# Kernel optimization log

Hardware: AMD Instinct MI355X
Metric: run time of the kernel (lower is better)

Reference implementation:

```python
import jax, jax.numpy as jnp
import numpy as np

N_NODES = 100000


def setup_inputs() -> dict:
    key = jax.random.key(0)
    ks = jax.random.split(key, 8)
    IN, HID, OUT = 128, 128, 64
    E = 1600000
    x = jax.random.normal(ks[0], (N_NODES, IN), dtype=jnp.float32)
    edge_index = jax.random.randint(ks[1], (2, E), 0, N_NODES, dtype=jnp.int64)
    # PyG SAGEConv params: lin_l (applied to aggregated neighbors, with bias),
    # lin_r (root weight, no bias).
    def lin(k, fi, fo):
        return jax.random.normal(k, (fi, fo), dtype=jnp.float32) / np.sqrt(fi)
    Wl0 = lin(ks[2], IN, HID)
    bl0 = jnp.zeros((HID,), dtype=jnp.float32)
    Wr0 = lin(ks[3], IN, HID)
    Wl1 = lin(ks[4], HID, OUT)
    bl1 = jnp.zeros((OUT,), dtype=jnp.float32)
    Wr1 = lin(ks[5], HID, OUT)
    return {"x": x, "edge_index": edge_index,
            "Wl0": Wl0, "bl0": bl0, "Wr0": Wr0,
            "Wl1": Wl1, "bl1": bl1, "Wr1": Wr1}


def _sage_conv(h, src, dst, Wl, bl, Wr):
    # mean aggregation of source features onto target nodes
    summed = jax.ops.segment_sum(h[src], dst, num_segments=N_NODES)  # [N, d]
    cnt = jax.ops.segment_sum(jnp.ones((src.shape[0], 1), h.dtype), dst,
                              num_segments=N_NODES)                  # [N, 1]
    agg = summed / jnp.maximum(cnt, 1.0)
    return agg @ Wl + bl + h @ Wr


def reference(x, edge_index, Wl0, bl0, Wr0, Wl1, bl1, Wr1):
    src, dst = edge_index[0], edge_index[1]
    h = jax.nn.relu(_sage_conv(x, src, dst, Wl0, bl0, Wr0))
    # dropout is identity in eval mode (training=False)
    return _sage_conv(h, src, dst, Wl1, bl1, Wr1)
```

## Files before the change

kernel.cpp:

```cpp
#include <hip/hip_runtime.h>


typedef short short8 __attribute__((ext_vector_type(8)));
typedef float f32x4 __attribute__((ext_vector_type(4)));
typedef float f32x2 __attribute__((ext_vector_type(2)));

#define NBUCK 782
#define BCAP  3072
#define EPB   8192

static __device__ __forceinline__ unsigned short f2bf(float f) {
    union { float f; unsigned u; } c; c.f = f;
    unsigned u = c.u + 0x7fffu + ((c.u >> 16) & 1u);
    return (unsigned short)(u >> 16);
}
static __device__ __forceinline__ float bf2f(unsigned short b) {
    union { unsigned u; float f; } c; c.u = ((unsigned)b) << 16;
    return c.f;
}
static __device__ __forceinline__ float bf2f_s(short b) {
    return bf2f((unsigned short)b);
}

static __device__ __forceinline__ unsigned char f2fp8(float x) {
    union { float f; unsigned u; } c; c.f = x;
    unsigned s = (c.u >> 24) & 0x80u;
    float a = __builtin_fabsf(x);
    if (a < 0.015625f) {
        int m = (int)rintf(a * 512.0f);
        return (unsigned char)(s | (unsigned)m);
    }
    unsigned u = c.u + 0x7ffffu + ((c.u >> 20) & 1u);
    int e = (int)((u >> 23) & 0xff) - 120;
    unsigned m = (u >> 20) & 7u;
    if (e > 15) { e = 15; m = 6; }
    return (unsigned char)(s | (unsigned)(e << 3) | m);
}

static __device__ __forceinline__ void acc_fp8x4(unsigned w, float* a) {
#if __has_builtin(__builtin_amdgcn_cvt_pk_f32_fp8)
    f32x2 lo = __builtin_amdgcn_cvt_pk_f32_fp8((int)w, false);
    f32x2 hi = __builtin_amdgcn_cvt_pk_f32_fp8((int)w, true);
    a[0] += lo[0]; a[1] += lo[1]; a[2] += hi[0]; a[3] += hi[1];
#else
    #pragma unroll
    for (int j = 0; j < 4; ++j) {
        unsigned b = (w >> (8 * j)) & 0xffu;
        union { unsigned u; float f; } c;
        c.u = ((b & 0x80u) << 24) | ((b & 0x7fu) << 20);
        a[j] += c.f * 0x1p120f;
    }
#endif
}
static __device__ __forceinline__ void acc_row16(uint4 w, float* a) {
    acc_fp8x4(w.x, a + 0);  acc_fp8x4(w.y, a + 4);
    acc_fp8x4(w.z, a + 8);  acc_fp8x4(w.w, a + 12);
}

__global__ __launch_bounds__(256) void k_pack(const float* __restrict__ WA,
                                              const float* __restrict__ WB,
                                              int CA, int NC,
                                              unsigned short* __restrict__ Wp) {
    int tid = blockIdx.x * 256 + threadIdx.x;
    if (tid >= NC * 16) return;
    int lane = tid & 63, kk = (tid >> 6) & 3, tg = tid >> 8;
    int l15 = lane & 15, quad = lane >> 4;
    int c = tg * 16 + l15;
    const float* W = (c < CA) ? WA : WB;
    int cc = (c < CA) ? c : c - CA;
    short8 v;
    #pragma unroll
    for (int j = 0; j < 8; ++j) {
        int k = kk * 32 + quad * 8 + j;
        v[j] = (short)f2bf(W[(size_t)k * CA + cc]);
    }
    *(short8*)(Wp + (size_t)tid * 8) = v;
}

__global__ __launch_bounds__(256) void k_gemm0_bucket(
        const float* __restrict__ X, const unsigned short* __restrict__ Wp,
        unsigned char* __restrict__ P0, unsigned short* __restrict__ Q0, int Nrows,
        const int* __restrict__ src, const int* __restrict__ dst,
        int* __restrict__ cursor, int* __restrict__ bregion,
        int E, int gemmBlocks) {
    const int t = threadIdx.x;
    if ((int)blockIdx.x < gemmBlocks) {
        const int wave = t >> 6, lane = t & 63;
        const int quad = lane >> 4, l15 = lane & 15;
        const int row0 = blockIdx.x * 32;
        const int c0w = wave * 64;
        f32x4 acc[2][4];
        #pragma unroll
        for (int mt = 0; mt < 2; ++mt)
            #pragma unroll
            for (int tt = 0; tt < 4; ++tt) acc[mt][tt] = (f32x4){0.f, 0.f, 0.f, 0.f};
        #pragma unroll
        for (int kk = 0; kk < 4; ++kk) {
            const int k0 = kk * 32 + quad * 8;
            short8 a[2];
            #pragma unroll
            for (int mt = 0; mt < 2; ++mt) {
                int row = row0 + mt * 16 + l15;
                if (row > Nrows - 1) row = Nrows - 1;
                const float* xp = X + (size_t)row * 128 + k0;
                float4 f0 = *(const float4*)xp;
                float4 f1 = *(const float4*)(xp + 4);
                short8 v;
                v[0] = (short)f2bf(f0.x); v[1] = (short)f2bf(f0.y);
                v[2] = (short)f2bf(f0.z); v[3] = (short)f2bf(f0.w);
                v[4] = (short)f2bf(f1.x); v[5] = (short)f2bf(f1.y);
                v[6] = (short)f2bf(f1.z); v[7] = (short)f2bf(f1.w);
                a[mt] = v;
            }
            short8 b[4];
            #pragma unroll
            for (int tt = 0; tt < 4; ++tt) {
                int tg = (c0w >> 4) + tt;
                b[tt] = *(const short8*)(Wp + ((size_t)(tg * 4 + kk) * 64 + lane) * 8);
            }
            #pragma unroll
            for (int mt = 0; mt < 2; ++mt)
                #pragma unroll
                for (int tt = 0; tt < 4; ++tt)
                    acc[mt][tt] = __builtin_amdgcn_mfma_f32_16x16x32_bf16(
                        a[mt], b[tt], acc[mt][tt], 0, 0, 0);
        }
        #pragma unroll
        for (int mt = 0; mt < 2; ++mt)
            #pragma unroll
            for (int r = 0; r < 4; ++r) {
                int row = row0 + mt * 16 + quad * 4 + r;
                if (row < Nrows) {
                    if (c0w < 128) {
                        #pragma unroll
                        for (int tt = 0; tt < 4; ++tt)
                            P0[(size_t)row * 128 + c0w + tt * 16 + l15] =
                                f2fp8(acc[mt][tt][r]);
                    } else {
                        #pragma unroll
                        for (int tt = 0; tt < 4; ++tt)
                            Q0[(size_t)row * 128 + (c0w - 128) + tt * 16 + l15] =
                                f2bf(acc[mt][tt][r]);
                    }
                }
            }
        return;
    }
    __shared__ int hist[NBUCK];
    __shared__ int basel[NBUCK];
    int bid = blockIdx.x - gemmBlocks;
    for (int i = t; i < NBUCK; i += 256) hist[i] = 0;
    __syncthreads();
    int e0 = bid * EPB + t * 32;
    int d[32];
    if (e0 + 32 <= E) {
        #pragma unroll
        for (int q = 0; q < 8; ++q) {
            int4 v = *(const int4*)(dst + e0 + q * 4);
            d[q * 4 + 0] = v.x; d[q * 4 + 1] = v.y;
            d[q * 4 + 2] = v.z; d[q * 4 + 3] = v.w;
        }
    } else {
        #pragma unroll
        for (int j = 0; j < 32; ++j) d[j] = (e0 + j < E) ? dst[e0 + j] : -1;
    }
    #pragma unroll
    for (int j = 0; j < 32; ++j)
        if (d[j] >= 0) atomicAdd(&hist[d[j] >> 7], 1);
    __syncthreads();
    for (int i = t; i < NBUCK; i += 256) {
        int c = hist[i];
        basel[i] = (c > 0) ? atomicAdd(&cursor[i], c) : 0;
    }
    __syncthreads();
    for (int i = t; i < NBUCK; i += 256) hist[i] = 0;
    __syncthreads();
    int s[32];
    if (e0 + 32 <= E) {
        #pragma unroll
        for (int q = 0; q < 8; ++q) {
            int4 v = *(const int4*)(src + e0 + q * 4);
            s[q * 4 + 0] = v.x; s[q * 4 + 1] = v.y;
            s[q * 4 + 2] = v.z; s[q * 4 + 3] = v.w;
        }
    } else {
        #pragma unroll
        for (int j = 0; j < 32; ++j) s[j] = (e0 + j < E) ? src[e0 + j] : 0;
    }
    #pragma unroll
    for (int j = 0; j < 32; ++j) {
        if (d[j] < 0) continue;
        int b = d[j] >> 7;
        int r = atomicAdd(&hist[b], 1);
        bregion[(size_t)b * BCAP + basel[b] + r] = s[j] | ((d[j] & 127) << 20);
    }
}

__global__ __launch_bounds__(256) void k_csr(const int* __restrict__ cursor,
                                             const int* __restrict__ bregion,
                                             int* __restrict__ rowptr,
                                             int* __restrict__ csr, int Nn) {
    __shared__ int words[BCAP];
    __shared__ int hist[128], sc[128], rank[128];
    __shared__ int red[256];
    int b = blockIdx.x, t = threadIdx.x;
    int part = 0;
    for (int i = t; i < b; i += 256) part += cursor[i];
    red[t] = part;
    if (t < 128) { hist[t] = 0; rank[t] = 0; }
    __syncthreads();
    #pragma unroll
    for (int off = 128; off > 0; off >>= 1) {
        if (t < off) red[t] += red[t + off];
        __syncthreads();
    }
    int gbase = red[0];
    int cnt = cursor[b];
    for (int i = t; i < cnt; i += 256) {
        int w = bregion[(size_t)b * BCAP + i];
        words[i] = w;
        atomicAdd(&hist[w >> 20], 1);
    }
    __syncthreads();
    if (t < 128) sc[t] = hist[t];
    __syncthreads();
    #pragma unroll
    for (int off = 1; off < 128; off <<= 1) {
        int x = 0;
        if (t < 128 && t >= off) x = sc[t - off];
        __syncthreads();
        if (t < 128) sc[t] += x;
        __syncthreads();
    }
    if (t < 128) sc[t] -= hist[t];
    __syncthreads();
    if (t < 128) {
        int node = b * 128 + t;
        if (node <= Nn) rowptr[node] = gbase + sc[t];
    }
    for (int i = t; i < cnt; i += 256) {
        int w = words[i];
        int d7 = w >> 20;
        int r = atomicAdd(&rank[d7], 1);
        csr[gbase + sc[d7] + r] = w & 0xFFFFF;
    }
}

__global__ __launch_bounds__(256) void k_gemm1(const unsigned short* __restrict__ Xv,
                                               const unsigned short* __restrict__ Wp,
                                               unsigned char* __restrict__ P1,
                                               unsigned short* __restrict__ Q1,
                                               int Nrows) {
    const int t = threadIdx.x;
    const int wave = t >> 6, lane = t & 63;
    const int quad = lane >> 4, l15 = lane & 15;
    const int row0 = blockIdx.x * 32;
    const int c0w = wave * 32;
    f32x4 acc[2][2];
    #pragma unroll
    for (int mt = 0; mt < 2; ++mt)
        #pragma unroll
        for (int tt = 0; tt < 2; ++tt) acc[mt][tt] = (f32x4){0.f, 0.f, 0.f, 0.f};
    #pragma unroll
    for (int kk = 0; kk < 4; ++kk) {
        const int k0 = kk * 32 + quad * 8;
        short8 a[2];
        #pragma unroll
        for (int mt = 0; mt < 2; ++mt) {
            int row = row0 + mt * 16 + l15;
            if (row > Nrows - 1) row = Nrows - 1;
            a[mt] = *(const short8*)(Xv + (size_t)row * 128 + k0);
        }
        short8 b[2];
        #pragma unroll
        for (int tt = 0; tt < 2; ++tt) {
            int tg = (c0w >> 4) + tt;
            b[tt] = *(const short8*)(Wp + ((size_t)(tg * 4 + kk) * 64 + lane) * 8);
        }
        #pragma unroll
        for (int mt = 0; mt < 2; ++mt)
            #pragma unroll
            for (int tt = 0; tt < 2; ++tt)
                acc[mt][tt] = __builtin_amdgcn_mfma_f32_16x16x32_bf16(
                    a[mt], b[tt], acc[mt][tt], 0, 0, 0);
    }
    #pragma unroll
    for (int mt = 0; mt < 2; ++mt)
        #pragma unroll
        for (int r = 0; r < 4; ++r) {
            int row = row0 + mt * 16 + quad * 4 + r;
            if (row < Nrows) {
                if (c0w < 64) {
                    #pragma unroll
                    for (int tt = 0; tt < 2; ++tt)
                        P1[(size_t)row * 64 + c0w + tt * 16 + l15] =
                            f2fp8(acc[mt][tt][r]);
                } else {
                    #pragma unroll
                    for (int tt = 0; tt < 2; ++tt)
                        Q1[(size_t)row * 64 + (c0w - 64) + tt * 16 + l15] =
                            f2bf(acc[mt][tt][r]);
                }
            }
        }
}

__global__ __launch_bounds__(256) void k_agg0(const unsigned char* __restrict__ P0,
                                              const unsigned short* __restrict__ Q0,
                                              const int* __restrict__ rowptr,
                                              const int* __restrict__ csr,
                                              const float* __restrict__ bl0,
                                              unsigned short* __restrict__ h, int Nn) {
    int wave = threadIdx.x >> 6, lane = threadIdx.x & 63;
    int g = lane >> 3, l7 = lane & 7;
    int n = (blockIdx.x * 4 + wave) * 8 + g;
    bool live = (n < Nn);
    int st = 0, dg = 0;
    if (live) { st = rowptr[n]; dg = rowptr[n + 1] - st; }
    float acc[16] = {};
    int e = 0;
    for (; e + 2 <= dg; e += 2) {
        int s0 = csr[st + e];
        int s1 = csr[st + e + 1];
        uint4 w0 = *(const uint4*)(P0 + (size_t)s0 * 128 + l7 * 16);
        uint4 w1 = *(const uint4*)(P0 + (size_t)s1 * 128 + l7 * 16);
        acc_row16(w0, acc);
        acc_row16(w1, acc);
    }
    if (e < dg) {
        int s0 = csr[st + e];
        uint4 w0 = *(const uint4*)(P0 + (size_t)s0 * 128 + l7 * 16);
        acc_row16(w0, acc);
    }
    if (live) {
        float inv = 1.f / fmaxf((float)dg, 1.f);
        short8 q0 = *(const short8*)(Q0 + (size_t)n * 128 + l7 * 16);
        short8 q1 = *(const short8*)(Q0 + (size_t)n * 128 + l7 * 16 + 8);
        float bb[16];
        *(float4*)(bb + 0)  = *(const float4*)(bl0 + l7 * 16);
        *(float4*)(bb + 4)  = *(const float4*)(bl0 + l7 * 16 + 4);
        *(float4*)(bb + 8)  = *(const float4*)(bl0 + l7 * 16 + 8);
        *(float4*)(bb + 12) = *(const float4*)(bl0 + l7 * 16 + 12);
        short8 o0, o1;
        #pragma unroll
        for (int j = 0; j < 8; ++j)
            o0[j] = (short)f2bf(fmaxf(acc[j] * inv + bb[j] + bf2f_s(q0[j]), 0.f));
        #pragma unroll
        for (int j = 0; j < 8; ++j)
            o1[j] = (short)f2bf(fmaxf(acc[8 + j] * inv + bb[8 + j] + bf2f_s(q1[j]), 0.f));
        *(short8*)(h + (size_t)n * 128 + l7 * 16) = o0;
        *(short8*)(h + (size_t)n * 128 + l7 * 16 + 8) = o1;
    }
}

__global__ __launch_bounds__(256) void k_agg1(const unsigned char* __restrict__ P1,
                                              const unsigned short* __restrict__ Q1,
                                              const int* __restrict__ rowptr,
                                              const int* __restrict__ csr,
                                              const float* __restrict__ bl1,
                                              float* __restrict__ out, int Nn) {
    int wave = threadIdx.x >> 6, lane = threadIdx.x & 63;
    int g = lane >> 2, l3 = lane & 3;
    int n = (blockIdx.x * 4 + wave) * 16 + g;
    bool live = (n < Nn);
    int st = 0, dg = 0;
    if (live) { st = rowptr[n]; dg = rowptr[n + 1] - st; }
    float acc[16] = {};
    int e = 0;
    for (; e + 2 <= dg; e += 2) {
        int s0 = csr[st + e];
        int s1 = csr[st + e + 1];
        uint4 w0 = *(const uint4*)(P1 + (size_t)s0 * 64 + l3 * 16);
        uint4 w1 = *(const uint4*)(P1 + (size_t)s1 * 64 + l3 * 16);
        acc_row16(w0, acc);
        acc_row16(w1, acc);
    }
    if (e < dg) {
        int s0 = csr[st + e];
        uint4 w0 = *(const uint4*)(P1 + (size_t)s0 * 64 + l3 * 16);
        acc_row16(w0, acc);
    }
    if (live) {
        float inv = 1.f / fmaxf((float)dg, 1.f);
        short8 q0 = *(const short8*)(Q1 + (size_t)n * 64 + l3 * 16);
        short8 q1 = *(const short8*)(Q1 + (size_t)n * 64 + l3 * 16 + 8);
        float bb[16];
        *(float4*)(bb + 0)  = *(const float4*)(bl1 + l3 * 16);
        *(float4*)(bb + 4)  = *(const float4*)(bl1 + l3 * 16 + 4);
        *(float4*)(bb + 8)  = *(const float4*)(bl1 + l3 * 16 + 8);
        *(float4*)(bb + 12) = *(const float4*)(bl1 + l3 * 16 + 12);
        float4 o[4];
        #pragma unroll
        for (int j = 0; j < 8; ++j)
            ((float*)o)[j] = acc[j] * inv + bb[j] + bf2f_s(q0[j]);
        #pragma unroll
        for (int j = 0; j < 8; ++j)
            ((float*)o)[8 + j] = acc[8 + j] * inv + bb[8 + j] + bf2f_s(q1[j]);
        #pragma unroll
        for (int q = 0; q < 4; ++q)
            *(float4*)(out + (size_t)n * 64 + l3 * 16 + q * 4) = o[q];
    }
}

extern "C" void kernel_launch(void* const* d_in, const int* in_sizes, int n_in,
                              void* d_out, int out_size, void* d_ws, size_t ws_size,
                              hipStream_t stream) {
    const float* x   = (const float*)d_in[0];
    const int* eidx  = (const int*)d_in[1];
    const float* Wl0 = (const float*)d_in[2];
    const float* bl0 = (const float*)d_in[3];
    const float* Wr0 = (const float*)d_in[4];
    const float* Wl1 = (const float*)d_in[5];
    const float* bl1 = (const float*)d_in[6];
    const float* Wr1 = (const float*)d_in[7];
    float* out = (float*)d_out;

    const int N = in_sizes[0] / 128;
    const int E = in_sizes[1] / 2;
    const int* src = eidx;
    const int* dst = eidx + E;

    int* rowptr  = (int*)d_ws;
    int* cursor  = rowptr + (N + 4);
    int* bregion = cursor + 784;
    int* csr     = bregion + (size_t)NBUCK * BCAP;
    unsigned short* Wp0 = (unsigned short*)(csr + E);
    unsigned short* Wp1 = Wp0 + 32768;
    unsigned char*  P0  = (unsigned char*)(Wp1 + 16384);
    unsigned short* Q0  = (unsigned short*)(P0 + (size_t)N * 128);
    unsigned short* h   = Q0 + (size_t)N * 128;
    unsigned char*  P1  = (unsigned char*)(h + (size_t)N * 128);
    unsigned short* Q1  = (unsigned short*)(P1 + (size_t)N * 64);

    hipMemsetAsync(cursor, 0, NBUCK * sizeof(int), stream);

    k_pack<<<(256 * 16 + 255) / 256, 256, 0, stream>>>(Wl0, Wr0, 128, 256, Wp0);
    k_pack<<<(128 * 16 + 255) / 256, 256, 0, stream>>>(Wl1, Wr1, 64, 128, Wp1);

    int gemmBlocks = (N + 31) / 32;
    int nbb = (E + EPB - 1) / EPB;
    k_gemm0_bucket<<<gemmBlocks + nbb, 256, 0, stream>>>(
        x, Wp0, P0, Q0, N, src, dst, cursor, bregion, E, gemmBlocks);
    k_csr<<<NBUCK, 256, 0, stream>>>(cursor, bregion, rowptr, csr, N);

    k_agg0<<<(N + 31) / 32, 256, 0, stream>>>(P0, Q0, rowptr, csr, bl0, h, N);
    k_gemm1<<<(N + 31) / 32, 256, 0, stream>>>(h, Wp1, P1, Q1, N);
    k_agg1<<<(N + 63) / 64, 256, 0, stream>>>(P1, Q1, rowptr, csr, bl1, out, N);
}
```

Before: 297.7 us.

## Fuse prep launches, reorder bucket blocks first, single-pass bucketing, unroll gathers

Merges the cursor memset and the two weight-pack launches into one prep kernel to cut launch overhead. Moves the edge-bucketing blocks to the front of the fused gemm/bucket grid, halves edges per thread, and records local ranks from the first histogram pass so the second atomic pass and the reload of src are gone. Both aggregation kernels now unroll the neighbor gather by four so more loads are in flight. The cost is more registers per thread and a different order of edges within each bucket.

```diff
diff --git a/kernel.cpp b/kernel.cpp
--- a/kernel.cpp
+++ b/kernel.cpp
@@ -7,7 +7,8 @@
 
 #define NBUCK 782
 #define BCAP  3072
-#define EPB   8192
+#define EPT   16
+#define EPB   4096
 
 static __device__ __forceinline__ unsigned short f2bf(float f) {
     union { float f; unsigned u; } c; c.f = f;
@@ -57,12 +58,10 @@
     acc_fp8x4(w.z, a + 8);  acc_fp8x4(w.w, a + 12);
 }
 
-__global__ __launch_bounds__(256) void k_pack(const float* __restrict__ WA,
-                                              const float* __restrict__ WB,
-                                              int CA, int NC,
-                                              unsigned short* __restrict__ Wp) {
-    int tid = blockIdx.x * 256 + threadIdx.x;
-    if (tid >= NC * 16) return;
+static __device__ __forceinline__ void pack_one(const float* __restrict__ WA,
+                                                const float* __restrict__ WB,
+                                                int CA, unsigned short* __restrict__ Wp,
+                                                int tid) {
     int lane = tid & 63, kk = (tid >> 6) & 3, tg = tid >> 8;
     int l15 = lane & 15, quad = lane >> 4;
     int c = tg * 16 + l15;
@@ -77,17 +76,32 @@
     *(short8*)(Wp + (size_t)tid * 8) = v;
 }
 
+__global__ __launch_bounds__(256) void k_prep(const float* __restrict__ Wl0,
+                                              const float* __restrict__ Wr0,
+                                              const float* __restrict__ Wl1,
+                                              const float* __restrict__ Wr1,
+                                              unsigned short* __restrict__ Wp0,
+                                              unsigned short* __restrict__ Wp1,
+                                              int* __restrict__ cursor) {
+    int tid = blockIdx.x * 256 + threadIdx.x;
+    if (blockIdx.x == 0) {
+        for (int i = threadIdx.x; i < NBUCK; i += 256) cursor[i] = 0;
+    }
+    if (tid < 4096) pack_one(Wl0, Wr0, 128, Wp0, tid);
+    else if (tid < 6144) pack_one(Wl1, Wr1, 64, Wp1, tid - 4096);
+}
+
 __global__ __launch_bounds__(256) void k_gemm0_bucket(
         const float* __restrict__ X, const unsigned short* __restrict__ Wp,
         unsigned char* __restrict__ P0, unsigned short* __restrict__ Q0, int Nrows,
         const int* __restrict__ src, const int* __restrict__ dst,
         int* __restrict__ cursor, int* __restrict__ bregion,
-        int E, int gemmBlocks) {
+        int E, int nbb) {
     const int t = threadIdx.x;
-    if ((int)blockIdx.x < gemmBlocks) {
+    if ((int)blockIdx.x >= nbb) {
         const int wave = t >> 6, lane = t & 63;
         const int quad = lane >> 4, l15 = lane & 15;
-        const int row0 = blockIdx.x * 32;
+        const int row0 = (blockIdx.x - nbb) * 32;
         const int c0w = wave * 64;
         f32x4 acc[2][4];
         #pragma unroll
@@ -148,51 +162,42 @@
     }
     __shared__ int hist[NBUCK];
     __shared__ int basel[NBUCK];
-    int bid = blockIdx.x - gemmBlocks;
+    int bid = blockIdx.x;
     for (int i = t; i < NBUCK; i += 256) hist[i] = 0;
     __syncthreads();
-    int e0 = bid * EPB + t * 32;
-    int d[32];
-    if (e0 + 32 <= E) {
-        #pragma unroll
-        for (int q = 0; q < 8; ++q) {
+    int e0 = bid * EPB + t * EPT;
+    int d[EPT], s[EPT], r[EPT];
+    if (e0 + EPT <= E) {
+        #pragma unroll
+        for (int q = 0; q < EPT / 4; ++q) {
             int4 v = *(const int4*)(dst + e0 + q * 4);
             d[q * 4 + 0] = v.x; d[q * 4 + 1] = v.y;
             d[q * 4 + 2] = v.z; d[q * 4 + 3] = v.w;
+            int4 w = *(const int4*)(src + e0 + q * 4);
+            s[q * 4 + 0] = w.x; s[q * 4 + 1] = w.y;
+            s[q * 4 + 2] = w.z; s[q * 4 + 3] = w.w;
         }
     } else {
         #pragma unroll
-        for (int j = 0; j < 32; ++j) d[j] = (e0 + j < E) ? dst[e0 + j] : -1;
-    }
-    #pragma unroll
-    for (int j = 0; j < 32; ++j)
-        if (d[j] >= 0) atomicAdd(&hist[d[j] >> 7], 1);
+        for (int j = 0; j < EPT; ++j) {
+            d[j] = (e0 + j < E) ? dst[e0 + j] : -1;
+            s[j] = (e0 + j < E) ? src[e0 + j] : 0;
+        }
+    }
+    #pragma unroll
+    for (int j = 0; j < EPT; ++j)
+        if (d[j] >= 0) r[j] = atomicAdd(&hist[d[j] >> 7], 1);
     __syncthreads();
     for (int i = t; i < NBUCK; i += 256) {
         int c = hist[i];
         basel[i] = (c > 0) ? atomicAdd(&cursor[i], c) : 0;
     }
     __syncthreads();
-    for (int i = t; i < NBUCK; i += 256) hist[i] = 0;
-    __syncthreads();
-    int s[32];
-    if (e0 + 32 <= E) {
-        #pragma unroll
-        for (int q = 0; q < 8; ++q) {
-            int4 v = *(const int4*)(src + e0 + q * 4);
-            s[q * 4 + 0] = v.x; s[q * 4 + 1] = v.y;
-            s[q * 4 + 2] = v.z; s[q * 4 + 3] = v.w;
-        }
-    } else {
-        #pragma unroll
-        for (int j = 0; j < 32; ++j) s[j] = (e0 + j < E) ? src[e0 + j] : 0;
-    }
-    #pragma unroll
-    for (int j = 0; j < 32; ++j) {
+    #pragma unroll
+    for (int j = 0; j < EPT; ++j) {
         if (d[j] < 0) continue;
         int b = d[j] >> 7;
-        int r = atomicAdd(&hist[b], 1);
-        bregion[(size_t)b * BCAP + basel[b] + r] = s[j] | ((d[j] & 127) << 20);
+        bregion[(size_t)b * BCAP + basel[b] + r[j]] = s[j] | ((d[j] & 127) << 20);
     }
 }
 
@@ -319,15 +324,17 @@
     if (live) { st = rowptr[n]; dg = rowptr[n + 1] - st; }
     float acc[16] = {};
     int e = 0;
-    for (; e + 2 <= dg; e += 2) {
-        int s0 = csr[st + e];
-        int s1 = csr[st + e + 1];
+    for (; e + 4 <= dg; e += 4) {
+        int s0 = csr[st + e], s1 = csr[st + e + 1];
+        int s2 = csr[st + e + 2], s3 = csr[st + e + 3];
         uint4 w0 = *(const uint4*)(P0 + (size_t)s0 * 128 + l7 * 16);
         uint4 w1 = *(const uint4*)(P0 + (size_t)s1 * 128 + l7 * 16);
-        acc_row16(w0, acc);
-        acc_row16(w1, acc);
-    }
-    if (e < dg) {
+        uint4 w2 = *(const uint4*)(P0 + (size_t)s2 * 128 + l7 * 16);
+        uint4 w3 = *(const uint4*)(P0 + (size_t)s3 * 128 + l7 * 16);
+        acc_row16(w0, acc); acc_row16(w1, acc);
+        acc_row16(w2, acc); acc_row16(w3, acc);
+    }
+    for (; e < dg; ++e) {
         int s0 = csr[st + e];
         uint4 w0 = *(const uint4*)(P0 + (size_t)s0 * 128 + l7 * 16);
         acc_row16(w0, acc);
@@ -367,15 +374,17 @@
     if (live) { st = rowptr[n]; dg = rowptr[n + 1] - st; }
     float acc[16] = {};
     int e = 0;
-    for (; e + 2 <= dg; e += 2) {
-        int s0 = csr[st + e];
-        int s1 = csr[st + e + 1];
+    for (; e + 4 <= dg; e += 4) {
+        int s0 = csr[st + e], s1 = csr[st + e + 1];
+        int s2 = csr[st + e + 2], s3 = csr[st + e + 3];
         uint4 w0 = *(const uint4*)(P1 + (size_t)s0 * 64 + l3 * 16);
         uint4 w1 = *(const uint4*)(P1 + (size_t)s1 * 64 + l3 * 16);
-        acc_row16(w0, acc);
-        acc_row16(w1, acc);
-    }
-    if (e < dg) {
+        uint4 w2 = *(const uint4*)(P1 + (size_t)s2 * 64 + l3 * 16);
+        uint4 w3 = *(const uint4*)(P1 + (size_t)s3 * 64 + l3 * 16);
+        acc_row16(w0, acc); acc_row16(w1, acc);
+        acc_row16(w2, acc); acc_row16(w3, acc);
+    }
+    for (; e < dg; ++e) {
         int s0 = csr[st + e];
         uint4 w0 = *(const uint4*)(P1 + (size_t)s0 * 64 + l3 * 16);
         acc_row16(w0, acc);
@@ -432,15 +441,12 @@
     unsigned char*  P1  = (unsigned char*)(h + (size_t)N * 128);
     unsigned short* Q1  = (unsigned short*)(P1 + (size_t)N * 64);
 
-    hipMemsetAsync(cursor, 0, NBUCK * sizeof(int), stream);
-
-    k_pack<<<(256 * 16 + 255) / 256, 256, 0, stream>>>(Wl0, Wr0, 128, 256, Wp0);
-    k_pack<<<(128 * 16 + 255) / 256, 256, 0, stream>>>(Wl1, Wr1, 64, 128, Wp1);
+    k_prep<<<24, 256, 0, stream>>>(Wl0, Wr0, Wl1, Wr1, Wp0, Wp1, cursor);
 
     int gemmBlocks = (N + 31) / 32;
     int nbb = (E + EPB - 1) / EPB;
-    k_gemm0_bucket<<<gemmBlocks + nbb, 256, 0, stream>>>(
-        x, Wp0, P0, Q0, N, src, dst, cursor, bregion, E, gemmBlocks);
+    k_gemm0_bucket<<<nbb + gemmBlocks, 256, 0, stream>>>(
+        x, Wp0, P0, Q0, N, src, dst, cursor, bregion, E, nbb);
     k_csr<<<NBUCK, 256, 0, stream>>>(cursor, bregion, rowptr, csr, N);
 
     k_agg0<<<(N + 31) / 32, 256, 0, stream>>>(P0, Q0, rowptr, csr, bl0, h, N);
```

Result: no change. 298.5 us (+0.3%).
